# Performance work log

Measured on AMD Instinct MI355X. Metric: run time of the kernel, lower is better.

## Reference

```python
import jax, jax.numpy as jnp
import numpy as np

B, S, D = 8, 4096, 1024
CAPACITY = 0.75
K = max(1, int(S * CAPACITY))  # 3072


def setup_inputs() -> dict:
    key = jax.random.key(0)
    k1, k2, k3 = jax.random.split(key, 3)
    x = jax.random.normal(k1, (B, S, D), dtype=jnp.float32)
    processed = jax.random.normal(k2, (B, K, D), dtype=jnp.float32)
    w_router = jax.random.normal(k3, (D,), dtype=jnp.float32) * 0.02
    return {"x": x, "processed": processed, "w_router": w_router}


def reference(x, processed, w_router):
    # --- MoDRouter.forward ---
    bsz, seq_len, dim = x.shape
    k = processed.shape[1]
    # scores: (B, S) = Linear(dim -> 1, no bias)
    scores = jnp.einsum('bsd,d->bs', x, w_router)
    # top-k per batch row, sorted descending (matches torch.topk sorted=True)
    topk_scores, indices = jax.lax.top_k(scores, k)  # (B, K)
    # gather routed tokens: (B, K, D)
    routed_x = jnp.take_along_axis(x, indices[:, :, None], axis=1)
    # --- MoDRouter.scatter_back (processed = block output for routed tokens) ---
    weights = jax.nn.softmax(topk_scores, axis=1)[:, :, None]  # (B, K, 1)
    # original values at routed positions == routed_x (same gather)
    blended = processed * weights + (1.0 - weights) * routed_x  # (B, K, D)
    batch_idx = jnp.arange(bsz)[:, None]  # (B, 1)
    output = x.at[batch_idx, indices].set(blended)  # unrouted positions keep x
    return output
```

## Files before the change

kernel.cpp:

```cpp
#include <hip/hip_runtime.h>
#include <math.h>

#define BB 8
#define SS 4096
#define DD 1024
#define KK 3072
#define NELEM (BB * SS)

typedef unsigned long long u64;
typedef unsigned int u32;
typedef float f32x4 __attribute__((ext_vector_type(4)));

__global__ __launch_bounds__(256) void mod_scores(const float* __restrict__ x,
                                                  const float* __restrict__ w,
                                                  float* __restrict__ scores,
                                                  u64* __restrict__ keys) {
    int wave = (int)((blockIdx.x * blockDim.x + threadIdx.x) >> 6);
    int lane = threadIdx.x & 63;
    if (wave >= NELEM) return;
    const float4* xr = (const float4*)(x + (size_t)wave * DD);
    const float4* wr = (const float4*)w;
    float acc = 0.f;
#pragma unroll
    for (int i = 0; i < 4; ++i) {
        float4 a = xr[lane + 64 * i];
        float4 b = wr[lane + 64 * i];
        acc += a.x * b.x + a.y * b.y + a.z * b.z + a.w * b.w;
    }
#pragma unroll
    for (int off = 32; off > 0; off >>= 1)
        acc += __shfl_down(acc, off, 64);
    if (lane == 0) {
        scores[wave] = acc;
        u32 u = __float_as_uint(acc);
        u32 m = (u & 0x80000000u) ? ~u : (u | 0x80000000u);
        keys[wave] = ((u64)(~m) << 32) | (u32)(wave & (SS - 1));
    }
}

__global__ __launch_bounds__(256) void mod_rank(const u64* __restrict__ keys,
                                                const float* __restrict__ scores,
                                                int* __restrict__ rank_of,
                                                float* __restrict__ partial) {
    __shared__ __align__(16) u64 lk[SS];
    __shared__ float red[256];
    const int ob = blockIdx.x;
    const int tid = threadIdx.x;
    const int gid = ob * 256 + tid;
    const int b = gid >> 12;
    const int lane = tid & 63;

    const u64* __restrict__ kb = keys + ((size_t)b << 12);
#pragma unroll
    for (int i = 0; i < 8; ++i) {
        int idx = tid + 256 * i;
        *(ulonglong2*)&lk[2 * idx] = *(const ulonglong2*)&kb[2 * idx];
    }
    __syncthreads();

    const u64 my = keys[gid];
    const u32 my_hi = (u32)(my >> 32);
    const u32 my_lo = (u32)my;

    int v_cnt = 0;
#pragma unroll
    for (int g = 0; g < 8; ++g) {
        u64 mj[8];
#pragma unroll
        for (int j = 0; j < 8; ++j) {
            u32 h = (u32)__builtin_amdgcn_readlane((int)my_hi, g * 8 + j);
            u32 l = (u32)__builtin_amdgcn_readlane((int)my_lo, g * 8 + j);
            mj[j] = ((u64)h << 32) | l;
        }
        int cnt[8] = {0, 0, 0, 0, 0, 0, 0, 0};
        for (int cg = 0; cg < SS / 64; ++cg) {
            u64 cv = lk[cg * 64 + lane];
#pragma unroll
            for (int j = 0; j < 8; ++j)
                cnt[j] += (int)__popcll(__ballot(cv < mj[j]));
        }
#pragma unroll
        for (int j = 0; j < 8; ++j)
            v_cnt = (lane == g * 8 + j) ? cnt[j] : v_cnt;
    }
    rank_of[gid] = v_cnt;

    float e = (v_cnt < KK) ? expf(scores[gid]) : 0.f;
    red[tid] = e;
    __syncthreads();
    for (int off = 128; off > 0; off >>= 1) {
        if (tid < off) red[tid] += red[tid + off];
        __syncthreads();
    }
    if (tid == 0) partial[ob] = red[0];
}

__global__ __launch_bounds__(256) void mod_blend(const float* __restrict__ x,
                                                 const float* __restrict__ proc,
                                                 const int* __restrict__ rank_of,
                                                 const float* __restrict__ scores,
                                                 const float* __restrict__ partial,
                                                 float* __restrict__ out) {
    const int row = blockIdx.x;
    const int b = row >> 12;
    const int t = threadIdx.x;
    const f32x4* xr = (const f32x4*)(x + (size_t)row * DD);
    f32x4* orow = (f32x4*)(out + (size_t)row * DD);
    const int j = rank_of[row];
    f32x4 a = xr[t];
    if (j < KK) {
        float denom = 0.f;
#pragma unroll
        for (int i = 0; i < 16; ++i) denom += partial[b * 16 + i];
        float w = expf(scores[row]) / denom;
        const f32x4* pr = (const f32x4*)(proc + ((size_t)b * KK + j) * DD);
        f32x4 p = __builtin_nontemporal_load(pr + t);
        f32x4 o = p * w + (1.f - w) * a;
        __builtin_nontemporal_store(o, orow + t);
    } else {
        __builtin_nontemporal_store(a, orow + t);
    }
}

extern "C" void kernel_launch(void* const* d_in, const int* in_sizes, int n_in,
                              void* d_out, int out_size, void* d_ws, size_t ws_size,
                              hipStream_t stream) {
    const float* x    = (const float*)d_in[0];
    const float* proc = (const float*)d_in[1];
    const float* w    = (const float*)d_in[2];
    float* out = (float*)d_out;

    u64*   keys    = (u64*)d_ws;
    float* scores  = (float*)((char*)d_ws + NELEM * 8);
    int*   rank_of = (int*)((char*)d_ws + NELEM * 12);
    float* partial = (float*)((char*)d_ws + NELEM * 16);

    mod_scores<<<NELEM / 4, 256, 0, stream>>>(x, w, scores, keys);
    mod_rank  <<<NELEM / 256, 256, 0, stream>>>(keys, scores, rank_of, partial);
    mod_blend <<<NELEM, 256, 0, stream>>>(x, proc, rank_of, scores, partial, out);
}
```

Measured before the change: 113.5 us.

## Fuse score, rank and blend into one persistent kernel with atomic flag barriers

Replaces three kernel launches with a single 1024-block kernel that computes router scores, ranks tokens, reduces softmax partials and blends, using per-batch atomic counters with spin-waits in place of kernel boundaries. The rank step is split into 8 chunks of 512 candidates per block, so each block stages a small LDS tile and writes partial counts that are summed later. This removes launch gaps and lets the rank work spread over more blocks. The cost is that correctness depends on all 1024 blocks being co-resident (launch bounds of 4 blocks per CU), and it adds spin-wait overhead plus a memset of the flags.

```diff
diff --git a/kernel.cpp b/kernel.cpp
--- a/kernel.cpp
+++ b/kernel.cpp
@@ -5,120 +5,171 @@
 #define SS 4096
 #define DD 1024
 #define KK 3072
+#define NCHUNK 8
+#define CHUNK 512
 #define NELEM (BB * SS)
 
 typedef unsigned long long u64;
 typedef unsigned int u32;
 typedef float f32x4 __attribute__((ext_vector_type(4)));
 
-__global__ __launch_bounds__(256) void mod_scores(const float* __restrict__ x,
-                                                  const float* __restrict__ w,
-                                                  float* __restrict__ scores,
-                                                  u64* __restrict__ keys) {
-    int wave = (int)((blockIdx.x * blockDim.x + threadIdx.x) >> 6);
-    int lane = threadIdx.x & 63;
-    if (wave >= NELEM) return;
-    const float4* xr = (const float4*)(x + (size_t)wave * DD);
-    const float4* wr = (const float4*)w;
-    float acc = 0.f;
+#define OFF_KEYS    0
+#define OFF_SCORES  262144
+#define OFF_RANK    393216
+#define OFF_PCNT    524288
+#define OFF_PARTIAL 1572864
+#define OFF_FLAGS   1573888
+
+__global__ __launch_bounds__(256, 4) void mod_fused(
+    const float* __restrict__ x, const float* __restrict__ proc,
+    const float* __restrict__ w, float* __restrict__ out,
+    u64* __restrict__ keys, float* __restrict__ scores,
+    int* __restrict__ rank_of, int* __restrict__ pcnt,
+    float* __restrict__ partial, int* flags)
+{
+    __shared__ __align__(16) u64 lk[CHUNK];
+    __shared__ float red[256];
+    int* done  = flags;
+    int* rdone = flags + 8;
+    int* pdone = flags + 136;
+
+    const int bid  = blockIdx.x;
+    const int tid  = threadIdx.x;
+    const int lane = tid & 63;
+    const int wv   = tid >> 6;
+    const int row0  = bid * 32;
+    const int batch = row0 >> 12;
+
+    {
+        const float4* wr = (const float4*)w;
+        float4 wl[4];
 #pragma unroll
-    for (int i = 0; i < 4; ++i) {
-        float4 a = xr[lane + 64 * i];
-        float4 b = wr[lane + 64 * i];
-        acc += a.x * b.x + a.y * b.y + a.z * b.z + a.w * b.w;
-    }
+        for (int i = 0; i < 4; ++i) wl[i] = wr[lane + 64 * i];
+        for (int r = 0; r < 8; ++r) {
+            int row = row0 + wv * 8 + r;
+            const float4* xr = (const float4*)(x + (size_t)row * DD);
+            float acc = 0.f;
 #pragma unroll
-    for (int off = 32; off > 0; off >>= 1)
-        acc += __shfl_down(acc, off, 64);
-    if (lane == 0) {
-        scores[wave] = acc;
-        u32 u = __float_as_uint(acc);
-        u32 m = (u & 0x80000000u) ? ~u : (u | 0x80000000u);
-        keys[wave] = ((u64)(~m) << 32) | (u32)(wave & (SS - 1));
-    }
-}
-
-__global__ __launch_bounds__(256) void mod_rank(const u64* __restrict__ keys,
-                                                const float* __restrict__ scores,
-                                                int* __restrict__ rank_of,
-                                                float* __restrict__ partial) {
-    __shared__ __align__(16) u64 lk[SS];
-    __shared__ float red[256];
-    const int ob = blockIdx.x;
-    const int tid = threadIdx.x;
-    const int gid = ob * 256 + tid;
-    const int b = gid >> 12;
-    const int lane = tid & 63;
-
-    const u64* __restrict__ kb = keys + ((size_t)b << 12);
+            for (int i = 0; i < 4; ++i) {
+                float4 a = xr[lane + 64 * i];
+                float4 b = wl[i];
+                acc += a.x * b.x + a.y * b.y + a.z * b.z + a.w * b.w;
+            }
 #pragma unroll
-    for (int i = 0; i < 8; ++i) {
-        int idx = tid + 256 * i;
-        *(ulonglong2*)&lk[2 * idx] = *(const ulonglong2*)&kb[2 * idx];
+            for (int off = 32; off > 0; off >>= 1)
+                acc += __shfl_down(acc, off, 64);
+            if (lane == 0) {
+                scores[row] = acc;
+                u32 u = __float_as_uint(acc);
+                u32 m = (u & 0x80000000u) ? ~u : (u | 0x80000000u);
+                keys[row] = ((u64)(~m) << 32) | (u32)(row & (SS - 1));
+            }
+        }
     }
     __syncthreads();
+    if (tid == 0) {
+        __threadfence();
+        __hip_atomic_fetch_add(&done[batch], 1, __ATOMIC_RELEASE, __HIP_MEMORY_SCOPE_AGENT);
+    }
 
-    const u64 my = keys[gid];
-    const u32 my_hi = (u32)(my >> 32);
-    const u32 my_lo = (u32)my;
+    const int ob = bid >> 3;
+    const int c  = bid & 7;
+    const int b2 = ob >> 4;
+    if (tid == 0) {
+        while (__hip_atomic_load(&done[b2], __ATOMIC_ACQUIRE, __HIP_MEMORY_SCOPE_AGENT) < 128)
+            __builtin_amdgcn_s_sleep(8);
+    }
+    __syncthreads();
+    {
+        const u64* __restrict__ cand = keys + ((size_t)b2 << 12) + c * CHUNK;
+        *(ulonglong2*)&lk[tid * 2] = *(const ulonglong2*)&cand[tid * 2];
+        const int gid2 = ob * 256 + tid;
+        const u64 my = keys[gid2];
+        __syncthreads();
 
-    int v_cnt = 0;
+        const u32 my_hi = (u32)(my >> 32);
+        const u32 my_lo = (u32)my;
+        int v_cnt = 0;
 #pragma unroll
-    for (int g = 0; g < 8; ++g) {
-        u64 mj[8];
+        for (int g = 0; g < 8; ++g) {
+            u64 mj[8];
 #pragma unroll
-        for (int j = 0; j < 8; ++j) {
-            u32 h = (u32)__builtin_amdgcn_readlane((int)my_hi, g * 8 + j);
-            u32 l = (u32)__builtin_amdgcn_readlane((int)my_lo, g * 8 + j);
-            mj[j] = ((u64)h << 32) | l;
-        }
-        int cnt[8] = {0, 0, 0, 0, 0, 0, 0, 0};
-        for (int cg = 0; cg < SS / 64; ++cg) {
-            u64 cv = lk[cg * 64 + lane];
+            for (int j = 0; j < 8; ++j) {
+                u32 h = (u32)__builtin_amdgcn_readlane((int)my_hi, g * 8 + j);
+                u32 l = (u32)__builtin_amdgcn_readlane((int)my_lo, g * 8 + j);
+                mj[j] = ((u64)h << 32) | l;
+            }
+            int cnt[8] = {0, 0, 0, 0, 0, 0, 0, 0};
+#pragma unroll
+            for (int cg = 0; cg < CHUNK / 64; ++cg) {
+                u64 cv = lk[cg * 64 + lane];
+#pragma unroll
+                for (int j = 0; j < 8; ++j)
+                    cnt[j] += (int)__popcll(__ballot(cv < mj[j]));
+            }
 #pragma unroll
             for (int j = 0; j < 8; ++j)
-                cnt[j] += (int)__popcll(__ballot(cv < mj[j]));
+                v_cnt = (lane == g * 8 + j) ? cnt[j] : v_cnt;
         }
+        pcnt[c * NELEM + gid2] = v_cnt;
+    }
+    __syncthreads();
+    if (tid == 0) {
+        __threadfence();
+        __hip_atomic_fetch_add(&rdone[ob], 1, __ATOMIC_RELEASE, __HIP_MEMORY_SCOPE_AGENT);
+    }
+
+    if (bid < 128) {
+        if (tid == 0) {
+            while (__hip_atomic_load(&rdone[bid], __ATOMIC_ACQUIRE, __HIP_MEMORY_SCOPE_AGENT) < 8)
+                __builtin_amdgcn_s_sleep(8);
+        }
+        __syncthreads();
+        const int gid3 = bid * 256 + tid;
+        int rr = 0;
 #pragma unroll
-        for (int j = 0; j < 8; ++j)
-            v_cnt = (lane == g * 8 + j) ? cnt[j] : v_cnt;
+        for (int cc = 0; cc < NCHUNK; ++cc) rr += pcnt[cc * NELEM + gid3];
+        rank_of[gid3] = rr;
+
+        float e = (rr < KK) ? expf(scores[gid3]) : 0.f;
+        red[tid] = e;
+        __syncthreads();
+        for (int off = 128; off > 0; off >>= 1) {
+            if (tid < off) red[tid] += red[tid + off];
+            __syncthreads();
+        }
+        if (tid == 0) {
+            partial[bid] = red[0];
+            __threadfence();
+            __hip_atomic_fetch_add(&pdone[bid >> 4], 1, __ATOMIC_RELEASE, __HIP_MEMORY_SCOPE_AGENT);
+        }
     }
-    rank_of[gid] = v_cnt;
 
-    float e = (v_cnt < KK) ? expf(scores[gid]) : 0.f;
-    red[tid] = e;
+    if (tid == 0) {
+        while (__hip_atomic_load(&pdone[batch], __ATOMIC_ACQUIRE, __HIP_MEMORY_SCOPE_AGENT) < 16)
+            __builtin_amdgcn_s_sleep(8);
+    }
     __syncthreads();
-    for (int off = 128; off > 0; off >>= 1) {
-        if (tid < off) red[tid] += red[tid + off];
-        __syncthreads();
-    }
-    if (tid == 0) partial[ob] = red[0];
-}
-
-__global__ __launch_bounds__(256) void mod_blend(const float* __restrict__ x,
-                                                 const float* __restrict__ proc,
-                                                 const int* __restrict__ rank_of,
-                                                 const float* __restrict__ scores,
-                                                 const float* __restrict__ partial,
-                                                 float* __restrict__ out) {
-    const int row = blockIdx.x;
-    const int b = row >> 12;
-    const int t = threadIdx.x;
-    const f32x4* xr = (const f32x4*)(x + (size_t)row * DD);
-    f32x4* orow = (f32x4*)(out + (size_t)row * DD);
-    const int j = rank_of[row];
-    f32x4 a = xr[t];
-    if (j < KK) {
+    {
         float denom = 0.f;
 #pragma unroll
-        for (int i = 0; i < 16; ++i) denom += partial[b * 16 + i];
-        float w = expf(scores[row]) / denom;
-        const f32x4* pr = (const f32x4*)(proc + ((size_t)b * KK + j) * DD);
-        f32x4 p = __builtin_nontemporal_load(pr + t);
-        f32x4 o = p * w + (1.f - w) * a;
-        __builtin_nontemporal_store(o, orow + t);
-    } else {
-        __builtin_nontemporal_store(a, orow + t);
+        for (int i = 0; i < 16; ++i) denom += partial[batch * 16 + i];
+        for (int r = 0; r < 32; ++r) {
+            int row = row0 + r;
+            const f32x4* xr = (const f32x4*)(x + (size_t)row * DD);
+            f32x4* orow = (f32x4*)(out + (size_t)row * DD);
+            int j = rank_of[row];
+            f32x4 a = xr[tid];
+            if (j < KK) {
+                float wgt = expf(scores[row]) / denom;
+                const f32x4* pr = (const f32x4*)(proc + ((size_t)batch * KK + j) * DD);
+                f32x4 p = __builtin_nontemporal_load(pr + tid);
+                f32x4 o = p * wgt + (1.f - wgt) * a;
+                __builtin_nontemporal_store(o, orow + tid);
+            } else {
+                __builtin_nontemporal_store(a, orow + tid);
+            }
+        }
     }
 }
 
@@ -130,12 +181,14 @@
     const float* w    = (const float*)d_in[2];
     float* out = (float*)d_out;
 
-    u64*   keys    = (u64*)d_ws;
-    float* scores  = (float*)((char*)d_ws + NELEM * 8);
-    int*   rank_of = (int*)((char*)d_ws + NELEM * 12);
-    float* partial = (float*)((char*)d_ws + NELEM * 16);
+    u64*   keys    = (u64*)((char*)d_ws + OFF_KEYS);
+    float* scores  = (float*)((char*)d_ws + OFF_SCORES);
+    int*   rank_of = (int*)((char*)d_ws + OFF_RANK);
+    int*   pcnt    = (int*)((char*)d_ws + OFF_PCNT);
+    float* partial = (float*)((char*)d_ws + OFF_PARTIAL);
+    int*   flags   = (int*)((char*)d_ws + OFF_FLAGS);
 
-    mod_scores<<<NELEM / 4, 256, 0, stream>>>(x, w, scores, keys);
-    mod_rank  <<<NELEM / 256, 256, 0, stream>>>(keys, scores, rank_of, partial);
-    mod_blend <<<NELEM, 256, 0, stream>>>(x, proc, rank_of, scores, partial, out);
+    hipMemsetAsync(flags, 0, 1024, stream);
+    mod_fused<<<1024, 256, 0, stream>>>(x, proc, w, out, keys, scores,
+                                        rank_of, pcnt, partial, flags);
 }
```

After: 298.2 us. 163% more time.

## Split rank comparisons across waves to quadruple rank-kernel block count

Applied to the files above, without the earlier changes.

The ranking kernel now assigns 64 elements per block and splits the 4096-key comparison loop across the block's four waves. Per-wave partial counts are summed in shared memory, and the softmax partial sums become per-64-element wave reductions. The aim is to fill more compute units than the previous 128-block launch. In exchange, every block reloads the full key array into LDS, and the blend kernel sums 64 partials per batch instead of 16.

```diff
diff --git a/kernel.cpp b/kernel.cpp
--- a/kernel.cpp
+++ b/kernel.cpp
@@ -38,19 +38,20 @@
     }
 }
 
-__global__ __launch_bounds__(256) void mod_rank(const u64* __restrict__ keys,
-                                                const float* __restrict__ scores,
-                                                int* __restrict__ rank_of,
-                                                float* __restrict__ partial) {
+__global__ __launch_bounds__(256) void mod_rank_full(const u64* __restrict__ keys,
+                                                     const float* __restrict__ scores,
+                                                     int* __restrict__ rank_of,
+                                                     float* __restrict__ partial) {
     __shared__ __align__(16) u64 lk[SS];
-    __shared__ float red[256];
-    const int ob = blockIdx.x;
-    const int tid = threadIdx.x;
-    const int gid = ob * 256 + tid;
-    const int b = gid >> 12;
+    __shared__ int redi[256];
+    const int bid  = blockIdx.x;
+    const int tid  = threadIdx.x;
     const int lane = tid & 63;
+    const int wv   = tid >> 6;
+    const int batch = bid >> 6;
+    const int gid0  = bid * 64;
 
-    const u64* __restrict__ kb = keys + ((size_t)b << 12);
+    const u64* __restrict__ kb = keys + ((size_t)batch << 12);
 #pragma unroll
     for (int i = 0; i < 8; ++i) {
         int idx = tid + 256 * i;
@@ -58,7 +59,7 @@
     }
     __syncthreads();
 
-    const u64 my = keys[gid];
+    const u64 my = lk[(bid & 63) * 64 + lane];
     const u32 my_hi = (u32)(my >> 32);
     const u32 my_lo = (u32)my;
 
@@ -73,8 +74,9 @@
             mj[j] = ((u64)h << 32) | l;
         }
         int cnt[8] = {0, 0, 0, 0, 0, 0, 0, 0};
-        for (int cg = 0; cg < SS / 64; ++cg) {
-            u64 cv = lk[cg * 64 + lane];
+#pragma unroll
+        for (int cg = 0; cg < 16; ++cg) {
+            u64 cv = lk[wv * 1024 + cg * 64 + lane];
 #pragma unroll
             for (int j = 0; j < 8; ++j)
                 cnt[j] += (int)__popcll(__ballot(cv < mj[j]));
@@ -83,16 +85,18 @@
         for (int j = 0; j < 8; ++j)
             v_cnt = (lane == g * 8 + j) ? cnt[j] : v_cnt;
     }
-    rank_of[gid] = v_cnt;
+    redi[tid] = v_cnt;
+    __syncthreads();
 
-    float e = (v_cnt < KK) ? expf(scores[gid]) : 0.f;
-    red[tid] = e;
-    __syncthreads();
-    for (int off = 128; off > 0; off >>= 1) {
-        if (tid < off) red[tid] += red[tid + off];
-        __syncthreads();
+    if (wv == 0) {
+        int r = redi[lane] + redi[64 + lane] + redi[128 + lane] + redi[192 + lane];
+        rank_of[gid0 + lane] = r;
+        float e = (r < KK) ? expf(scores[gid0 + lane]) : 0.f;
+#pragma unroll
+        for (int off = 32; off > 0; off >>= 1)
+            e += __shfl_down(e, off, 64);
+        if (lane == 0) partial[bid] = e;
     }
-    if (tid == 0) partial[ob] = red[0];
 }
 
 __global__ __launch_bounds__(256) void mod_blend(const float* __restrict__ x,
@@ -111,7 +115,7 @@
     if (j < KK) {
         float denom = 0.f;
 #pragma unroll
-        for (int i = 0; i < 16; ++i) denom += partial[b * 16 + i];
+        for (int i = 0; i < 64; ++i) denom += partial[b * 64 + i];
         float w = expf(scores[row]) / denom;
         const f32x4* pr = (const f32x4*)(proc + ((size_t)b * KK + j) * DD);
         f32x4 p = __builtin_nontemporal_load(pr + t);
@@ -135,7 +139,7 @@
     int*   rank_of = (int*)((char*)d_ws + NELEM * 12);
     float* partial = (float*)((char*)d_ws + NELEM * 16);
 
-    mod_scores<<<NELEM / 4, 256, 0, stream>>>(x, w, scores, keys);
-    mod_rank  <<<NELEM / 256, 256, 0, stream>>>(keys, scores, rank_of, partial);
-    mod_blend <<<NELEM, 256, 0, stream>>>(x, proc, rank_of, scores, partial, out);
+    mod_scores   <<<NELEM / 4, 256, 0, stream>>>(x, w, scores, keys);
+    mod_rank_full<<<NELEM / 64, 256, 0, stream>>>(keys, scores, rank_of, partial);
+    mod_blend    <<<NELEM, 256, 0, stream>>>(x, proc, rank_of, scores, partial, out);
 }
```

After: 95.23 us. 16.1% less time.
